# Optimization experiments

Hardware: AMD Instinct MI355X
Metric: run time of the kernel (lower is better)

The kernel has to match this reference:

```python
import jax, jax.numpy as jnp
import numpy as np

N_NODES = 100000
N_EDGES = 1600000
NFEAT = 128
NHID = 128
NS = 64
NCLASS = 16
B = 8192


def setup_inputs() -> dict:
    key = jax.random.key(0)
    ks = jax.random.split(key, 12)
    s = jax.random.normal(ks[0], (B, NS), dtype=jnp.float32)
    x = jax.random.normal(ks[1], (N_NODES, NFEAT), dtype=jnp.float32)
    row = jax.random.randint(ks[2], (N_EDGES,), 0, N_NODES)
    col = jax.random.randint(ks[3], (N_EDGES,), 0, N_NODES)
    val = jax.random.uniform(ks[4], (N_EDGES,), dtype=jnp.float32)
    index = jax.random.randint(ks[5], (B,), 0, N_NODES)
    # learned parameters (glorot-ish scale)
    W1 = jax.random.normal(ks[6], (NFEAT, NHID), dtype=jnp.float32) / np.sqrt(NFEAT)
    b1 = jnp.zeros((NHID,), dtype=jnp.float32)
    W2 = jax.random.normal(ks[7], (NHID, NHID), dtype=jnp.float32) / np.sqrt(NHID)
    b2 = jnp.zeros((NHID,), dtype=jnp.float32)
    Wl = jax.random.normal(ks[8], (NHID + NS, NCLASS), dtype=jnp.float32) / np.sqrt(NHID + NS)
    bl = jnp.zeros((NCLASS,), dtype=jnp.float32)
    return {"s": s, "x": x, "row": row, "col": col, "val": val,
            "index": index, "W1": W1, "b1": b1, "W2": W2, "b2": b2,
            "Wl": Wl, "bl": bl}


def reference(s, x, row, col, val, index, W1, b1, W2, b2, Wl, bl):
    n = x.shape[0]

    def spmm(h):
        # adj @ h with adj in COO form: out[r] += val_e * h[c]
        return jax.ops.segment_sum(val[:, None] * h[col], row, num_segments=n)

    # dropout is identity in eval mode (training=False)
    h = jax.nn.relu(spmm(x @ W1) + b1)          # gc1 + relu
    h = spmm(h @ W2) + b2                        # gc2
    z = jnp.concatenate([h[index], s], axis=1) @ Wl + bl  # [B, nclass]
    return jax.nn.log_softmax(z, axis=1)
```

## Files before the change

kernel.cpp:

```cpp
#include <hip/hip_runtime.h>
#include <math.h>

#define N_NODES 100000
#define N_EDGES 1600000
#define NFEAT 128
#define NHID 128
#define NS 64
#define NCLASS 16
#define BB 8192

#define B1_SHIFT 11
#define NB1 49
#define SUB_SHIFT 5
#define NSUB 3125
#define CHUNK 1024
#define HWG 256
#define SUB_NB 13

typedef unsigned long long ull;
typedef unsigned int uint;


__device__ __forceinline__ unsigned short f2bf(float f) {
  unsigned int u = __float_as_uint(f);
  return (unsigned short)((u + 0x7fffu + ((u >> 16) & 1u)) >> 16);
}
__device__ __forceinline__ float bflo(unsigned int u) {
  return __uint_as_float(u << 16);
}
__device__ __forceinline__ float bfhi(unsigned int u) {
  return __uint_as_float(u & 0xffff0000u);
}
__device__ __forceinline__ unsigned int packbf2(float lo, float hi) {
  return (unsigned int)f2bf(lo) | ((unsigned int)f2bf(hi) << 16);
}


__device__ __forceinline__ ull pack_edge(float v, int r, int c) {
  return ((ull)(__float_as_uint(v) >> 2) << 34) | ((ull)(unsigned)r << 17) | (unsigned)c;
}
__device__ __forceinline__ int edge_col(ull p) { return (int)(p & 0x1FFFFu); }
__device__ __forceinline__ int edge_row(ull p) { return (int)((unsigned)(p >> 17) & 0x1FFFFu); }
__device__ __forceinline__ float edge_val(ull p) {
  return __uint_as_float(((unsigned)(p >> 34)) << 2);
}


__global__ __launch_bounds__(256) void histsub_kernel(const int* __restrict__ row,
                                                      int* __restrict__ part_hist) {
  __shared__ int lh[NSUB];
  int tid = threadIdx.x;
  for (int i = tid; i < NSUB; i += 256) lh[i] = 0;
  __syncthreads();
  for (long i = (long)blockIdx.x * 256 + tid; i < N_EDGES; i += (long)HWG * 256)
    atomicAdd(&lh[row[i] >> SUB_SHIFT], 1);
  __syncthreads();
  int* dst = part_hist + blockIdx.x * NSUB;
  for (int i = tid; i < NSUB; i += 256) dst[i] = lh[i];
}

__global__ __launch_bounds__(256) void reduce_kernel(const int* __restrict__ part_hist,
                                                     int* __restrict__ subcnt) {
  int b = blockIdx.x * 256 + threadIdx.x;
  if (b >= NSUB) return;
  int s = 0;
  for (int w = 0; w < HWG; ++w) s += part_hist[w * NSUB + b];
  subcnt[b] = s;
}


__global__ __launch_bounds__(256) void partial2_kernel(const int* __restrict__ subcnt,
                                                       int* __restrict__ bsum) {
  __shared__ int sd[256];
  int i = blockIdx.x * 256 + threadIdx.x;
  sd[threadIdx.x] = (i < NSUB) ? subcnt[i] : 0;
  __syncthreads();
  for (int o = 128; o > 0; o >>= 1) {
    if (threadIdx.x < o) sd[threadIdx.x] += sd[threadIdx.x + o];
    __syncthreads();
  }
  if (threadIdx.x == 0) bsum[blockIdx.x] = sd[0];
}

__global__ __launch_bounds__(64) void scanp2_kernel(const int* __restrict__ bsum,
                                                    int* __restrict__ bpre,
                                                    int* __restrict__ sub_offs) {
  int tid = threadIdx.x;
  int v = (tid < SUB_NB) ? bsum[tid] : 0;
  int x = v;
  for (int o = 1; o < 64; o <<= 1) {
    int y = __shfl_up(x, o);
    if (tid >= o) x += y;
  }
  if (tid < SUB_NB) bpre[tid] = x - v;
  if (tid == SUB_NB - 1) sub_offs[NSUB] = x;
}

__global__ __launch_bounds__(256) void apply2_kernel(const int* __restrict__ subcnt,
                                                     const int* __restrict__ bpre,
                                                     int* __restrict__ sub_offs) {
  __shared__ int sd[256];
  int tid = threadIdx.x;
  int i = blockIdx.x * 256 + tid;
  int v = (i < NSUB) ? subcnt[i] : 0;
  sd[tid] = v;
  __syncthreads();
  for (int o = 1; o < 256; o <<= 1) {
    int add = (tid >= o) ? sd[tid - o] : 0;
    __syncthreads();
    sd[tid] += add;
    __syncthreads();
  }
  if (i < NSUB) sub_offs[i] = bpre[blockIdx.x] + sd[tid] - v;
}

__global__ __launch_bounds__(256) void initcur_kernel(const int* __restrict__ sub_offs,
                                                      int* __restrict__ gcur1,
                                                      int* __restrict__ gcur2) {
  int t = blockIdx.x * 256 + threadIdx.x;
  if (t < NB1) gcur1[t] = sub_offs[t << 6];
  if (t < NSUB) gcur2[t] = sub_offs[t];
}


__global__ __launch_bounds__(256) void binA_kernel(const int* __restrict__ row,
                                                   const int* __restrict__ col,
                                                   const float* __restrict__ val,
                                                   int* __restrict__ gcur1,
                                                   ull* __restrict__ ebuf1) {
  __shared__ ull stage[CHUNK];
  __shared__ int hist[NB1], lofs[NB1 + 1], lcur[NB1], gbase[NB1];
  int tid = threadIdx.x;
  for (long base = (long)blockIdx.x * CHUNK; base < N_EDGES; base += (long)gridDim.x * CHUNK) {
    int cnt = (int)min((long)CHUNK, (long)N_EDGES - base);
    if (tid < NB1) hist[tid] = 0;
    __syncthreads();
    ull e[4]; int bk[4];
#pragma unroll
    for (int v = 0; v < 4; ++v) {
      int i = v * 256 + tid;
      bk[v] = -1;
      if (i < cnt) {
        long g = base + i;
        int r = row[g];
        e[v] = pack_edge(val[g], r, col[g]);
        bk[v] = r >> B1_SHIFT;
        atomicAdd(&hist[bk[v]], 1);
      }
    }
    __syncthreads();
    if (tid < 64) {
      int h = (tid < NB1) ? hist[tid] : 0;
      int x = h;
      for (int o = 1; o < 64; o <<= 1) {
        int y = __shfl_up(x, o);
        if (tid >= o) x += y;
      }
      if (tid < NB1) { lofs[tid] = x - h; lcur[tid] = x - h; }
      if (tid == 63) lofs[NB1] = x;
    }
    __syncthreads();
#pragma unroll
    for (int v = 0; v < 4; ++v) {
      if (bk[v] >= 0) {
        int pos = atomicAdd(&lcur[bk[v]], 1);
        stage[pos] = e[v];
      }
    }
    __syncthreads();
    if (tid < NB1) {
      int h = hist[tid];
      if (h > 0) gbase[tid] = atomicAdd(&gcur1[tid], h);
    }
    __syncthreads();
    for (int s = tid; s < cnt; s += 256) {
      int lo = 0, hi = NB1;
      while (hi - lo > 1) {
        int mid = (lo + hi) >> 1;
        if (lofs[mid] <= s) lo = mid; else hi = mid;
      }
      ebuf1[gbase[lo] + (s - lofs[lo])] = stage[s];
    }
    __syncthreads();
  }
}


__global__ __launch_bounds__(256) void binB_kernel(const ull* __restrict__ ebuf1,
                                                   const int* __restrict__ sub_offs,
                                                   int* __restrict__ gcur2,
                                                   ull* __restrict__ edat) {
  __shared__ ull stage[CHUNK];
  __shared__ int hist[64], lofs[65], lcur[64], gbase[64];
  int tid = threadIdx.x;
  int b1 = blockIdx.x >> 3, w = blockIdx.x & 7;
  int rbeg = sub_offs[b1 << 6];
  int rend = sub_offs[min((b1 + 1) << 6, NSUB)];
  for (int base = rbeg + w * CHUNK; base < rend; base += 8 * CHUNK) {
    int cnt = min(CHUNK, rend - base);
    if (tid < 64) hist[tid] = 0;
    __syncthreads();
    ull e[4]; int bk[4];
#pragma unroll
    for (int v = 0; v < 4; ++v) {
      int i = v * 256 + tid;
      bk[v] = -1;
      if (i < cnt) {
        e[v] = ebuf1[base + i];
        bk[v] = (edge_row(e[v]) >> SUB_SHIFT) - (b1 << 6);
        atomicAdd(&hist[bk[v]], 1);
      }
    }
    __syncthreads();
    if (tid < 64) {
      int h = hist[tid];
      int x = h;
      for (int o = 1; o < 64; o <<= 1) {
        int y = __shfl_up(x, o);
        if (tid >= o) x += y;
      }
      lofs[tid] = x - h;
      lcur[tid] = x - h;
      if (tid == 63) lofs[64] = x;
    }
    __syncthreads();
#pragma unroll
    for (int v = 0; v < 4; ++v) {
      if (bk[v] >= 0) {
        int pos = atomicAdd(&lcur[bk[v]], 1);
        stage[pos] = e[v];
      }
    }
    __syncthreads();
    if (tid < 64) {
      int h = hist[tid];
      if (h > 0) gbase[tid] = atomicAdd(&gcur2[(b1 << 6) + tid], h);
    }
    __syncthreads();
    for (int s = tid; s < cnt; s += 256) {
      int lo = 0, hi = 64;
      while (hi - lo > 1) {
        int mid = (lo + hi) >> 1;
        if (lofs[mid] <= s) lo = mid; else hi = mid;
      }
      edat[gbase[lo] + (s - lofs[lo])] = stage[s];
    }
    __syncthreads();
  }
}


__global__ __launch_bounds__(256) void binC_kernel(const int* __restrict__ sub_offs,
                                                   ull* __restrict__ edat,
                                                   ull* __restrict__ ebuf1,
                                                   int* __restrict__ offs) {
  __shared__ int rcnt[32], rofs[32], rcur[32];
  int s = blockIdx.x, tid = threadIdx.x;
  int r0 = s << SUB_SHIFT;
  int beg = sub_offs[s], end = sub_offs[s + 1];
  int n = end - beg;
  if (tid < 32) rcnt[tid] = 0;
  __syncthreads();
  for (int i = tid; i < n; i += 256) {
    ull p = edat[beg + i];
    ebuf1[beg + i] = p;
    atomicAdd(&rcnt[edge_row(p) & 31], 1);
  }
  __syncthreads();
  if (tid < 32) {
    int h = rcnt[tid];
    int x = h;
    for (int o = 1; o < 32; o <<= 1) {
      int y = __shfl_up(x, o, 32);
      if (tid >= o) x += y;
    }
    rofs[tid] = x - h;
    rcur[tid] = x - h;
    offs[r0 + tid] = beg + x - h;
    if (s == NSUB - 1 && tid == 31) offs[N_NODES] = end;
  }
  __syncthreads();
  for (int i = tid; i < n; i += 256) {
    ull p = ebuf1[beg + i];
    int pos = atomicAdd(&rcur[edge_row(p) & 31], 1);
    edat[beg + pos] = p;
  }
}


__global__ __launch_bounds__(256) void mask_kernel(const int* __restrict__ offs,
                                                   const ull* __restrict__ edat,
                                                   const int* __restrict__ index,
                                                   int* __restrict__ flag) {
  int t = blockIdx.x * 256 + threadIdx.x;
  int r = index[t];
  int s = offs[r], e = offs[r + 1];
  for (int j = s; j < e; ++j) flag[edge_col(edat[j])] = 1;
}


__global__ __launch_bounds__(256) void wconv_kernel(const float* __restrict__ W,
                                                    uint* __restrict__ Wt) {
  int idx = blockIdx.x * 256 + threadIdx.x;
  int n = idx >> 6, kc = idx & 63;
  float lo = W[(2 * kc) * 128 + n];
  float hi = W[(2 * kc + 1) * 128 + n];
  Wt[idx] = packbf2(lo, hi);
}


typedef __attribute__((ext_vector_type(8))) __bf16 bf16x8;
typedef __attribute__((ext_vector_type(4))) float f32x4;
union FragU { uint4 u; bf16x8 b; };

#define LDSTR 68

template <int OUT_BF16>
__global__ __launch_bounds__(256) void mfma_gemm_kernel(const float* __restrict__ A,
                                                        const uint* __restrict__ Wt_g,
                                                        const float* __restrict__ bias,
                                                        void* __restrict__ C,
                                                        int nrows) {
  __shared__ uint As_s[64 * LDSTR];
  __shared__ uint Wt_s[128 * LDSTR];
  int tid = threadIdx.x;
  int rbase = blockIdx.x * 64;

  {
    const uint2* src = (const uint2*)Wt_g;
#pragma unroll
    for (int i = 0; i < 16; ++i) {
      int j = i * 256 + tid;
      int n = j >> 5, c2 = (j & 31) * 2;
      uint2 v = src[j];
      Wt_s[n * LDSTR + c2] = v.x;
      Wt_s[n * LDSTR + c2 + 1] = v.y;
    }
  }
  {
    const float4* src = (const float4*)(A + (long)rbase * 128);
#pragma unroll
    for (int i = 0; i < 8; ++i) {
      int f = i * 256 + tid;
      int m = f >> 5;
      float4 v = (rbase + m < nrows) ? src[f] : make_float4(0.f, 0.f, 0.f, 0.f);
      int c = (f & 31) * 2;
      As_s[m * LDSTR + c]     = packbf2(v.x, v.y);
      As_s[m * LDSTR + c + 1] = packbf2(v.z, v.w);
    }
  }
  __syncthreads();

  int w = tid >> 6, lane = tid & 63;
  int quad = lane >> 4, lr = lane & 15;
  int n0 = w * 32;

  f32x4 acc[4][2];
#pragma unroll
  for (int mt = 0; mt < 4; ++mt)
#pragma unroll
    for (int nt = 0; nt < 2; ++nt) acc[mt][nt] = (f32x4){0.f, 0.f, 0.f, 0.f};

#pragma unroll
  for (int kk = 0; kk < 4; ++kk) {
    int kc = kk * 16 + quad * 4;
    FragU fb0, fb1;
    fb0.u = *(const uint4*)&Wt_s[(n0 + lr) * LDSTR + kc];
    fb1.u = *(const uint4*)&Wt_s[(n0 + 16 + lr) * LDSTR + kc];
#pragma unroll
    for (int mt = 0; mt < 4; ++mt) {
      FragU fa;
      fa.u = *(const uint4*)&As_s[(mt * 16 + lr) * LDSTR + kc];
      acc[mt][0] = __builtin_amdgcn_mfma_f32_16x16x32_bf16(fa.b, fb0.b, acc[mt][0], 0, 0, 0);
      acc[mt][1] = __builtin_amdgcn_mfma_f32_16x16x32_bf16(fa.b, fb1.b, acc[mt][1], 0, 0, 0);
    }
  }

#pragma unroll
  for (int mt = 0; mt < 4; ++mt) {
#pragma unroll
    for (int nt = 0; nt < 2; ++nt) {
      int col = n0 + nt * 16 + lr;
      float bv = OUT_BF16 ? 0.f : bias[col];
#pragma unroll
      for (int r = 0; r < 4; ++r) {
        int row = rbase + mt * 16 + quad * 4 + r;
        if (row < nrows) {
          if (OUT_BF16)
            ((unsigned short*)C)[(long)row * 128 + col] = f2bf(acc[mt][nt][r]);
          else
            ((float*)C)[(long)row * 128 + col] = acc[mt][nt][r] + bv;
        }
      }
    }
  }
}


__global__ __launch_bounds__(256) void spmm_row_kernel(const int* __restrict__ offs,
                                                       const ull* __restrict__ edat,
                                                       const unsigned short* __restrict__ a,
                                                       const float* __restrict__ bias,
                                                       unsigned short* __restrict__ h,
                                                       const int* __restrict__ flag) {
  int wave = threadIdx.x >> 6;
  int lane = threadIdx.x & 63;
  int r = blockIdx.x * 4 + wave;
  if (!flag[r]) return;
  int g = lane >> 4, l = lane & 15;
  int s = offs[r], e = offs[r + 1];
  float acc[8] = {0.f, 0.f, 0.f, 0.f, 0.f, 0.f, 0.f, 0.f};
  for (int j = s + g; j < e; j += 4) {
    ull p = edat[j];
    float v = edge_val(p);
    uint4 u = *(const uint4*)(a + (long)edge_col(p) * 128 + l * 8);
    acc[0] = fmaf(v, bflo(u.x), acc[0]);
    acc[1] = fmaf(v, bfhi(u.x), acc[1]);
    acc[2] = fmaf(v, bflo(u.y), acc[2]);
    acc[3] = fmaf(v, bfhi(u.y), acc[3]);
    acc[4] = fmaf(v, bflo(u.z), acc[4]);
    acc[5] = fmaf(v, bfhi(u.z), acc[5]);
    acc[6] = fmaf(v, bflo(u.w), acc[6]);
    acc[7] = fmaf(v, bfhi(u.w), acc[7]);
  }
#pragma unroll
  for (int k = 0; k < 8; ++k) {
    acc[k] += __shfl_xor(acc[k], 16);
    acc[k] += __shfl_xor(acc[k], 32);
  }
  if (g == 0) {
    float4 b0 = *(const float4*)(bias + l * 8);
    float4 b1 = *(const float4*)(bias + l * 8 + 4);
    uint4 o;
    o.x = packbf2(fmaxf(acc[0] + b0.x, 0.f), fmaxf(acc[1] + b0.y, 0.f));
    o.y = packbf2(fmaxf(acc[2] + b0.z, 0.f), fmaxf(acc[3] + b0.w, 0.f));
    o.z = packbf2(fmaxf(acc[4] + b1.x, 0.f), fmaxf(acc[5] + b1.y, 0.f));
    o.w = packbf2(fmaxf(acc[6] + b1.z, 0.f), fmaxf(acc[7] + b1.w, 0.f));
    *(uint4*)(h + (long)r * 128 + l * 8) = o;
  }
}

__global__ __launch_bounds__(256) void spmm_sel_kernel(const int* __restrict__ offs,
                                                       const ull* __restrict__ edat,
                                                       const unsigned short* __restrict__ h1,
                                                       const int* __restrict__ index,
                                                       float* __restrict__ g2) {
  int wave = threadIdx.x >> 6;
  int lane = threadIdx.x & 63;
  int b = blockIdx.x * 4 + wave;
  int g = lane >> 4, l = lane & 15;
  int r = index[b];
  int s = offs[r], e = offs[r + 1];
  float acc[8] = {0.f, 0.f, 0.f, 0.f, 0.f, 0.f, 0.f, 0.f};
  for (int j = s + g; j < e; j += 4) {
    ull p = edat[j];
    float v = edge_val(p);
    uint4 u = *(const uint4*)(h1 + (long)edge_col(p) * 128 + l * 8);
    acc[0] = fmaf(v, bflo(u.x), acc[0]);
    acc[1] = fmaf(v, bfhi(u.x), acc[1]);
    acc[2] = fmaf(v, bflo(u.y), acc[2]);
    acc[3] = fmaf(v, bfhi(u.y), acc[3]);
    acc[4] = fmaf(v, bflo(u.z), acc[4]);
    acc[5] = fmaf(v, bfhi(u.z), acc[5]);
    acc[6] = fmaf(v, bflo(u.w), acc[6]);
    acc[7] = fmaf(v, bfhi(u.w), acc[7]);
  }
#pragma unroll
  for (int k = 0; k < 8; ++k) {
    acc[k] += __shfl_xor(acc[k], 16);
    acc[k] += __shfl_xor(acc[k], 32);
  }
  if (g == 0) {
    float* op = g2 + (long)b * 128 + l * 8;
    *(float4*)(op + 0) = make_float4(acc[0], acc[1], acc[2], acc[3]);
    *(float4*)(op + 4) = make_float4(acc[4], acc[5], acc[6], acc[7]);
  }
}


__global__ __launch_bounds__(128) void final_kernel(const float* __restrict__ t,
                                                    const float* __restrict__ s,
                                                    const float* __restrict__ Wl,
                                                    const float* __restrict__ bl,
                                                    float* __restrict__ out) {
  int b = blockIdx.x * 128 + threadIdx.x;
  float z[16];
#pragma unroll
  for (int c = 0; c < 16; ++c) z[c] = bl[c];
  const float4* tb = (const float4*)(t + (long)b * 128);
#pragma unroll 4
  for (int k4 = 0; k4 < 32; ++k4) {
    float4 tv = tb[k4];
    const float* w = Wl + (k4 * 4) * 16;
#pragma unroll
    for (int c = 0; c < 16; ++c)
      z[c] += tv.x * w[c] + tv.y * w[16 + c] + tv.z * w[32 + c] + tv.w * w[48 + c];
  }
  const float4* sb = (const float4*)(s + (long)b * 64);
#pragma unroll 4
  for (int k4 = 0; k4 < 16; ++k4) {
    float4 sv = sb[k4];
    const float* w = Wl + (128 + k4 * 4) * 16;
#pragma unroll
    for (int c = 0; c < 16; ++c)
      z[c] += sv.x * w[c] + sv.y * w[16 + c] + sv.z * w[32 + c] + sv.w * w[48 + c];
  }
  float m = z[0];
#pragma unroll
  for (int c = 1; c < 16; ++c) m = fmaxf(m, z[c]);
  float sum = 0.f;
#pragma unroll
  for (int c = 0; c < 16; ++c) sum += expf(z[c] - m);
  float lse = m + logf(sum);
  float* ob = out + (long)b * 16;
#pragma unroll
  for (int c = 0; c < 16; ++c) ob[c] = z[c] - lse;
}


extern "C" void kernel_launch(void* const* d_in, const int* in_sizes, int n_in,
                              void* d_out, int out_size, void* d_ws, size_t ws_size,
                              hipStream_t stream) {
  const float* s_in  = (const float*)d_in[0];
  const float* x     = (const float*)d_in[1];
  const int*   row   = (const int*)d_in[2];
  const int*   col   = (const int*)d_in[3];
  const float* val   = (const float*)d_in[4];
  const int*   index = (const int*)d_in[5];
  const float* W1    = (const float*)d_in[6];
  const float* b1    = (const float*)d_in[7];
  const float* W2    = (const float*)d_in[8];
  const float* b2    = (const float*)d_in[9];
  const float* Wl    = (const float*)d_in[10];
  const float* bl    = (const float*)d_in[11];
  float* out = (float*)d_out;

  ull* edat  = (ull*)d_ws;
  ull* ebuf1 = edat + N_EDGES;
  unsigned short* a  = (unsigned short*)(ebuf1 + N_EDGES);
  unsigned short* h1 = a + (size_t)N_NODES * 128;
  float* g2   = (float*)(h1 + (size_t)N_NODES * 128);
  float* tmat = g2 + (size_t)BB * 128;
  int* flag   = (int*)(tmat + (size_t)BB * 128);
  int* offs   = flag + N_NODES;
  int* sub_offs = offs + (N_NODES + 1);
  int* subcnt = sub_offs + (NSUB + 1);
  int* bsum2  = subcnt + NSUB;
  int* bpre2  = bsum2 + SUB_NB;
  int* gcur1  = bpre2 + SUB_NB;
  int* gcur2  = gcur1 + NB1;
  uint* Wt1   = (uint*)(gcur2 + NSUB);
  uint* Wt2   = Wt1 + 8192;
  int* part_hist = (int*)(Wt2 + 8192);

  hipMemsetAsync(flag, 0, N_NODES * sizeof(int), stream);

  histsub_kernel<<<HWG, 256, 0, stream>>>(row, part_hist);
  reduce_kernel<<<SUB_NB, 256, 0, stream>>>(part_hist, subcnt);
  partial2_kernel<<<SUB_NB, 256, 0, stream>>>(subcnt, bsum2);
  scanp2_kernel<<<1, 64, 0, stream>>>(bsum2, bpre2, sub_offs);
  apply2_kernel<<<SUB_NB, 256, 0, stream>>>(subcnt, bpre2, sub_offs);
  initcur_kernel<<<(NSUB + 255) / 256, 256, 0, stream>>>(sub_offs, gcur1, gcur2);

  binA_kernel<<<512, 256, 0, stream>>>(row, col, val, gcur1, ebuf1);
  binB_kernel<<<NB1 * 8, 256, 0, stream>>>(ebuf1, sub_offs, gcur2, edat);
  binC_kernel<<<NSUB, 256, 0, stream>>>(sub_offs, edat, ebuf1, offs);
  mask_kernel<<<BB / 256, 256, 0, stream>>>(offs, edat, index, flag);

  wconv_kernel<<<32, 256, 0, stream>>>(W1, Wt1);
  wconv_kernel<<<32, 256, 0, stream>>>(W2, Wt2);

  mfma_gemm_kernel<1><<<(N_NODES + 63) / 64, 256, 0, stream>>>(x, Wt1, nullptr, a, N_NODES);
  spmm_row_kernel<<<N_NODES / 4, 256, 0, stream>>>(offs, edat, a, b1, h1, flag);
  spmm_sel_kernel<<<BB / 4, 256, 0, stream>>>(offs, edat, h1, index, g2);
  mfma_gemm_kernel<0><<<BB / 64, 256, 0, stream>>>(g2, Wt2, b2, tmat, BB);
  final_kernel<<<BB / 128, 128, 0, stream>>>(tmat, s_in, Wl, bl, out);
}
```

Before: 350.2 us.

## Merge scan kernels, stage binC in LDS, fuse wconv, unroll SpMM loops

Replaces the per-block histogram dump plus reduce and three-stage scan with global atomics into subcnt and a single 1024-thread scan kernel that also initializes the cursors. binC now stages each sub-bucket in shared memory instead of round-tripping through a global buffer when it fits, with a fallback path for oversized buckets. The two weight-conversion launches are merged into one, and both SpMM gather loops are unrolled by two to keep more loads in flight. This cuts kernel launch count and global traffic in preprocessing, at the cost of global atomic contention in the histogram and a 16KB LDS allocation in binC.

```diff
diff --git a/kernel.cpp b/kernel.cpp
--- a/kernel.cpp
+++ b/kernel.cpp
@@ -15,7 +15,7 @@
 #define NSUB 3125
 #define CHUNK 1024
 #define HWG 256
-#define SUB_NB 13
+#define BINC_CAP 2048
 
 typedef unsigned long long ull;
 typedef unsigned int uint;
@@ -47,7 +47,7 @@
 
 
 __global__ __launch_bounds__(256) void histsub_kernel(const int* __restrict__ row,
-                                                      int* __restrict__ part_hist) {
+                                                      int* __restrict__ subcnt) {
   __shared__ int lh[NSUB];
   int tid = threadIdx.x;
   for (int i = tid; i < NSUB; i += 256) lh[i] = 0;
@@ -55,71 +55,48 @@
   for (long i = (long)blockIdx.x * 256 + tid; i < N_EDGES; i += (long)HWG * 256)
     atomicAdd(&lh[row[i] >> SUB_SHIFT], 1);
   __syncthreads();
-  int* dst = part_hist + blockIdx.x * NSUB;
-  for (int i = tid; i < NSUB; i += 256) dst[i] = lh[i];
-}
-
-__global__ __launch_bounds__(256) void reduce_kernel(const int* __restrict__ part_hist,
-                                                     int* __restrict__ subcnt) {
-  int b = blockIdx.x * 256 + threadIdx.x;
-  if (b >= NSUB) return;
-  int s = 0;
-  for (int w = 0; w < HWG; ++w) s += part_hist[w * NSUB + b];
-  subcnt[b] = s;
-}
-
-
-__global__ __launch_bounds__(256) void partial2_kernel(const int* __restrict__ subcnt,
-                                                       int* __restrict__ bsum) {
-  __shared__ int sd[256];
-  int i = blockIdx.x * 256 + threadIdx.x;
-  sd[threadIdx.x] = (i < NSUB) ? subcnt[i] : 0;
+  for (int i = tid; i < NSUB; i += 256) {
+    int c = lh[i];
+    if (c) atomicAdd(&subcnt[i], c);
+  }
+}
+
+
+__global__ __launch_bounds__(1024) void scanall_kernel(const int* __restrict__ subcnt,
+                                                       int* __restrict__ sub_offs,
+                                                       int* __restrict__ gcur1,
+                                                       int* __restrict__ gcur2) {
+  __shared__ int sd[1024];
+  int tid = threadIdx.x;
+  int b0 = tid * 4;
+  int vv[4];
+  int loc = 0;
+#pragma unroll
+  for (int k = 0; k < 4; ++k) {
+    int i = b0 + k;
+    vv[k] = (i < NSUB) ? subcnt[i] : 0;
+    loc += vv[k];
+  }
+  sd[tid] = loc;
   __syncthreads();
-  for (int o = 128; o > 0; o >>= 1) {
-    if (threadIdx.x < o) sd[threadIdx.x] += sd[threadIdx.x + o];
-    __syncthreads();
-  }
-  if (threadIdx.x == 0) bsum[blockIdx.x] = sd[0];
-}
-
-__global__ __launch_bounds__(64) void scanp2_kernel(const int* __restrict__ bsum,
-                                                    int* __restrict__ bpre,
-                                                    int* __restrict__ sub_offs) {
-  int tid = threadIdx.x;
-  int v = (tid < SUB_NB) ? bsum[tid] : 0;
-  int x = v;
-  for (int o = 1; o < 64; o <<= 1) {
-    int y = __shfl_up(x, o);
-    if (tid >= o) x += y;
-  }
-  if (tid < SUB_NB) bpre[tid] = x - v;
-  if (tid == SUB_NB - 1) sub_offs[NSUB] = x;
-}
-
-__global__ __launch_bounds__(256) void apply2_kernel(const int* __restrict__ subcnt,
-                                                     const int* __restrict__ bpre,
-                                                     int* __restrict__ sub_offs) {
-  __shared__ int sd[256];
-  int tid = threadIdx.x;
-  int i = blockIdx.x * 256 + tid;
-  int v = (i < NSUB) ? subcnt[i] : 0;
-  sd[tid] = v;
-  __syncthreads();
-  for (int o = 1; o < 256; o <<= 1) {
+  for (int o = 1; o < 1024; o <<= 1) {
     int add = (tid >= o) ? sd[tid - o] : 0;
     __syncthreads();
     sd[tid] += add;
     __syncthreads();
   }
-  if (i < NSUB) sub_offs[i] = bpre[blockIdx.x] + sd[tid] - v;
-}
-
-__global__ __launch_bounds__(256) void initcur_kernel(const int* __restrict__ sub_offs,
-                                                      int* __restrict__ gcur1,
-                                                      int* __restrict__ gcur2) {
-  int t = blockIdx.x * 256 + threadIdx.x;
-  if (t < NB1) gcur1[t] = sub_offs[t << 6];
-  if (t < NSUB) gcur2[t] = sub_offs[t];
+  int pre = sd[tid] - loc;
+#pragma unroll
+  for (int k = 0; k < 4; ++k) {
+    int i = b0 + k;
+    if (i < NSUB) {
+      sub_offs[i] = pre;
+      gcur2[i] = pre;
+      if ((i & 63) == 0) gcur1[i >> 6] = pre;
+      pre += vv[k];
+    }
+  }
+  if (tid == 1023) sub_offs[NSUB] = sd[1023];
 }
 
 
@@ -254,36 +231,62 @@
                                                    ull* __restrict__ edat,
                                                    ull* __restrict__ ebuf1,
                                                    int* __restrict__ offs) {
-  __shared__ int rcnt[32], rofs[32], rcur[32];
+  __shared__ ull es[BINC_CAP];
+  __shared__ int rcnt[32], rcur[32];
   int s = blockIdx.x, tid = threadIdx.x;
   int r0 = s << SUB_SHIFT;
   int beg = sub_offs[s], end = sub_offs[s + 1];
   int n = end - beg;
   if (tid < 32) rcnt[tid] = 0;
   __syncthreads();
-  for (int i = tid; i < n; i += 256) {
-    ull p = edat[beg + i];
-    ebuf1[beg + i] = p;
-    atomicAdd(&rcnt[edge_row(p) & 31], 1);
-  }
-  __syncthreads();
-  if (tid < 32) {
-    int h = rcnt[tid];
-    int x = h;
-    for (int o = 1; o < 32; o <<= 1) {
-      int y = __shfl_up(x, o, 32);
-      if (tid >= o) x += y;
-    }
-    rofs[tid] = x - h;
-    rcur[tid] = x - h;
-    offs[r0 + tid] = beg + x - h;
-    if (s == NSUB - 1 && tid == 31) offs[N_NODES] = end;
-  }
-  __syncthreads();
-  for (int i = tid; i < n; i += 256) {
-    ull p = ebuf1[beg + i];
-    int pos = atomicAdd(&rcur[edge_row(p) & 31], 1);
-    edat[beg + pos] = p;
+  if (n <= BINC_CAP) {
+    for (int i = tid; i < n; i += 256) {
+      ull p = edat[beg + i];
+      es[i] = p;
+      atomicAdd(&rcnt[edge_row(p) & 31], 1);
+    }
+    __syncthreads();
+    if (tid < 32) {
+      int h = rcnt[tid];
+      int x = h;
+      for (int o = 1; o < 32; o <<= 1) {
+        int y = __shfl_up(x, o, 32);
+        if (tid >= o) x += y;
+      }
+      rcur[tid] = x - h;
+      offs[r0 + tid] = beg + x - h;
+      if (s == NSUB - 1 && tid == 31) offs[N_NODES] = end;
+    }
+    __syncthreads();
+    for (int i = tid; i < n; i += 256) {
+      ull p = es[i];
+      int pos = atomicAdd(&rcur[edge_row(p) & 31], 1);
+      edat[beg + pos] = p;
+    }
+  } else {
+    for (int i = tid; i < n; i += 256) {
+      ull p = edat[beg + i];
+      ebuf1[beg + i] = p;
+      atomicAdd(&rcnt[edge_row(p) & 31], 1);
+    }
+    __syncthreads();
+    if (tid < 32) {
+      int h = rcnt[tid];
+      int x = h;
+      for (int o = 1; o < 32; o <<= 1) {
+        int y = __shfl_up(x, o, 32);
+        if (tid >= o) x += y;
+      }
+      rcur[tid] = x - h;
+      offs[r0 + tid] = beg + x - h;
+      if (s == NSUB - 1 && tid == 31) offs[N_NODES] = end;
+    }
+    __syncthreads();
+    for (int i = tid; i < n; i += 256) {
+      ull p = ebuf1[beg + i];
+      int pos = atomicAdd(&rcur[edge_row(p) & 31], 1);
+      edat[beg + pos] = p;
+    }
   }
 }
 
@@ -299,9 +302,14 @@
 }
 
 
-__global__ __launch_bounds__(256) void wconv_kernel(const float* __restrict__ W,
-                                                    uint* __restrict__ Wt) {
-  int idx = blockIdx.x * 256 + threadIdx.x;
+__global__ __launch_bounds__(256) void wconv2_kernel(const float* __restrict__ W1,
+                                                     const float* __restrict__ W2,
+                                                     uint* __restrict__ Wt1,
+                                                     uint* __restrict__ Wt2) {
+  int blk = blockIdx.x;
+  const float* W = (blk < 32) ? W1 : W2;
+  uint* Wt = (blk < 32) ? Wt1 : Wt2;
+  int idx = (blk & 31) * 256 + threadIdx.x;
   int n = idx >> 6, kc = idx & 63;
   float lo = W[(2 * kc) * 128 + n];
   float hi = W[(2 * kc + 1) * 128 + n];
@@ -396,6 +404,17 @@
   }
 }
 
+
+__device__ __forceinline__ void fma_row(float* acc, float v, uint4 u) {
+  acc[0] = fmaf(v, bflo(u.x), acc[0]);
+  acc[1] = fmaf(v, bfhi(u.x), acc[1]);
+  acc[2] = fmaf(v, bflo(u.y), acc[2]);
+  acc[3] = fmaf(v, bfhi(u.y), acc[3]);
+  acc[4] = fmaf(v, bflo(u.z), acc[4]);
+  acc[5] = fmaf(v, bfhi(u.z), acc[5]);
+  acc[6] = fmaf(v, bflo(u.w), acc[6]);
+  acc[7] = fmaf(v, bfhi(u.w), acc[7]);
+}
 
 __global__ __launch_bounds__(256) void spmm_row_kernel(const int* __restrict__ offs,
                                                        const ull* __restrict__ edat,
@@ -410,18 +429,19 @@
   int g = lane >> 4, l = lane & 15;
   int s = offs[r], e = offs[r + 1];
   float acc[8] = {0.f, 0.f, 0.f, 0.f, 0.f, 0.f, 0.f, 0.f};
-  for (int j = s + g; j < e; j += 4) {
+  int j = s + g;
+  for (; j + 4 < e; j += 8) {
+    ull p0 = edat[j];
+    ull p1 = edat[j + 4];
+    uint4 u0 = *(const uint4*)(a + (long)edge_col(p0) * 128 + l * 8);
+    uint4 u1 = *(const uint4*)(a + (long)edge_col(p1) * 128 + l * 8);
+    fma_row(acc, edge_val(p0), u0);
+    fma_row(acc, edge_val(p1), u1);
+  }
+  if (j < e) {
     ull p = edat[j];
-    float v = edge_val(p);
     uint4 u = *(const uint4*)(a + (long)edge_col(p) * 128 + l * 8);
-    acc[0] = fmaf(v, bflo(u.x), acc[0]);
-    acc[1] = fmaf(v, bfhi(u.x), acc[1]);
-    acc[2] = fmaf(v, bflo(u.y), acc[2]);
-    acc[3] = fmaf(v, bfhi(u.y), acc[3]);
-    acc[4] = fmaf(v, bflo(u.z), acc[4]);
-    acc[5] = fmaf(v, bfhi(u.z), acc[5]);
-    acc[6] = fmaf(v, bflo(u.w), acc[6]);
-    acc[7] = fmaf(v, bfhi(u.w), acc[7]);
+    fma_row(acc, edge_val(p), u);
   }
 #pragma unroll
   for (int k = 0; k < 8; ++k) {
@@ -452,18 +472,19 @@
   int r = index[b];
   int s = offs[r], e = offs[r + 1];
   float acc[8] = {0.f, 0.f, 0.f, 0.f, 0.f, 0.f, 0.f, 0.f};
-  for (int j = s + g; j < e; j += 4) {
+  int j = s + g;
+  for (; j + 4 < e; j += 8) {
+    ull p0 = edat[j];
+    ull p1 = edat[j + 4];
+    uint4 u0 = *(const uint4*)(h1 + (long)edge_col(p0) * 128 + l * 8);
+    uint4 u1 = *(const uint4*)(h1 + (long)edge_col(p1) * 128 + l * 8);
+    fma_row(acc, edge_val(p0), u0);
+    fma_row(acc, edge_val(p1), u1);
+  }
+  if (j < e) {
     ull p = edat[j];
-    float v = edge_val(p);
     uint4 u = *(const uint4*)(h1 + (long)edge_col(p) * 128 + l * 8);
-    acc[0] = fmaf(v, bflo(u.x), acc[0]);
-    acc[1] = fmaf(v, bfhi(u.x), acc[1]);
-    acc[2] = fmaf(v, bflo(u.y), acc[2]);
-    acc[3] = fmaf(v, bfhi(u.y), acc[3]);
-    acc[4] = fmaf(v, bflo(u.z), acc[4]);
-    acc[5] = fmaf(v, bfhi(u.z), acc[5]);
-    acc[6] = fmaf(v, bflo(u.w), acc[6]);
-    acc[7] = fmaf(v, bfhi(u.w), acc[7]);
+    fma_row(acc, edge_val(p), u);
   }
 #pragma unroll
   for (int k = 0; k < 8; ++k) {
@@ -542,33 +563,25 @@
   float* g2   = (float*)(h1 + (size_t)N_NODES * 128);
   float* tmat = g2 + (size_t)BB * 128;
   int* flag   = (int*)(tmat + (size_t)BB * 128);
-  int* offs   = flag + N_NODES;
+  int* subcnt = flag + N_NODES;
+  int* offs   = subcnt + NSUB;
   int* sub_offs = offs + (N_NODES + 1);
-  int* subcnt = sub_offs + (NSUB + 1);
-  int* bsum2  = subcnt + NSUB;
-  int* bpre2  = bsum2 + SUB_NB;
-  int* gcur1  = bpre2 + SUB_NB;
+  int* gcur1  = sub_offs + (NSUB + 1);
   int* gcur2  = gcur1 + NB1;
   uint* Wt1   = (uint*)(gcur2 + NSUB);
   uint* Wt2   = Wt1 + 8192;
-  int* part_hist = (int*)(Wt2 + 8192);
-
-  hipMemsetAsync(flag, 0, N_NODES * sizeof(int), stream);
-
-  histsub_kernel<<<HWG, 256, 0, stream>>>(row, part_hist);
-  reduce_kernel<<<SUB_NB, 256, 0, stream>>>(part_hist, subcnt);
-  partial2_kernel<<<SUB_NB, 256, 0, stream>>>(subcnt, bsum2);
-  scanp2_kernel<<<1, 64, 0, stream>>>(bsum2, bpre2, sub_offs);
-  apply2_kernel<<<SUB_NB, 256, 0, stream>>>(subcnt, bpre2, sub_offs);
-  initcur_kernel<<<(NSUB + 255) / 256, 256, 0, stream>>>(sub_offs, gcur1, gcur2);
+
+  hipMemsetAsync(flag, 0, (N_NODES + NSUB) * sizeof(int), stream);
+
+  histsub_kernel<<<HWG, 256, 0, stream>>>(row, subcnt);
+  scanall_kernel<<<1, 1024, 0, stream>>>(subcnt, sub_offs, gcur1, gcur2);
 
   binA_kernel<<<512, 256, 0, stream>>>(row, col, val, gcur1, ebuf1);
   binB_kernel<<<NB1 * 8, 256, 0, stream>>>(ebuf1, sub_offs, gcur2, edat);
   binC_kernel<<<NSUB, 256, 0, stream>>>(sub_offs, edat, ebuf1, offs);
   mask_kernel<<<BB / 256, 256, 0, stream>>>(offs, edat, index, flag);
 
-  wconv_kernel<<<32, 256, 0, stream>>>(W1, Wt1);
-  wconv_kernel<<<32, 256, 0, stream>>>(W2, Wt2);
+  wconv2_kernel<<<64, 256, 0, stream>>>(W1, W2, Wt1, Wt2);
 
   mfma_gemm_kernel<1><<<(N_NODES + 63) / 64, 256, 0, stream>>>(x, Wt1, nullptr, a, N_NODES);
   spmm_row_kernel<<<N_NODES / 4, 256, 0, stream>>>(offs, edat, a, b1, h1, flag);
```

After: 318.3 us. 9.1% less time.
